# Performance work log

Hardware: AMD Instinct MI355X
Metric: run time of the kernel (lower is better)

## Reference

```python
import jax, jax.numpy as jnp
import numpy as np

BATCH = 16384
STEPS = 32
LAT = 64
IN_W = STEPS * (2 * LAT + 1) + 2 * LAT  # 4256


def setup_inputs() -> dict:
    key = jax.random.key(0)
    k1, k2 = jax.random.split(key)
    inputs = jax.random.normal(k1, (BATCH, IN_W), dtype=jnp.float32) * 0.1
    noise = jax.random.normal(k2, (BATCH, LAT), dtype=jnp.float32)
    return {"inputs": inputs, "noise": noise, "flow_steps": STEPS, "latent_dim": LAT}


def reference(inputs, noise, flow_steps, latent_dim):
    S, L = flow_steps, latent_dim
    B = inputs.shape[0]
    q0_mu = inputs[:, :L]
    q0_logsigma2 = inputs[:, L:2 * L]
    z0 = q0_mu + noise * jnp.exp(0.5 * q0_logsigma2)  # reparam sample (B, L)
    # initial variational loss term (add_loss in original)
    kl0 = -0.5 * jnp.mean(jnp.sum(noise * noise, axis=-1) + jnp.sum(q0_logsigma2, axis=-1))
    # per-step flow params, laid out step-major for scan: (S, B, L) and (S, B)
    U = inputs[:, 2 * L:(2 + S) * L].reshape(B, S, L).transpose(1, 0, 2)
    W = inputs[:, (2 + S) * L:(2 + 2 * S) * L].reshape(B, S, L).transpose(1, 0, 2)
    b = inputs[:, (2 + 2 * S) * L:(2 + 2 * S) * L + S].T  # (S, B)

    def step(z, uwb):
        u, w, bb = uwb
        h = jnp.sum(w * z, axis=-1) + bb          # (B,)
        uw = jnp.sum(u * w, axis=-1)              # (B,)
        t = jnp.tanh(h)
        # log|det Jacobian| loss term (tanh activation branch)
        loss = -jnp.mean(jnp.log(jnp.abs((1.0 - t * t) * uw + 1.0)))
        z = z + u * t[:, None]
        return z, loss

    z, losses = jax.lax.scan(step, z0, (U, W, b))
    total_loss = kl0 + jnp.sum(losses)
    return z, total_loss
```

## Files before the change

kernel.cpp:

```cpp
#include <hip/hip_runtime.h>
#include <math.h>


constexpr int BATCH = 16384;
constexpr int STEPS = 32;
constexpr int LAT   = 64;
constexpr int IN_W  = STEPS * (2 * LAT + 1) + 2 * LAT;

template <int CTRL>
__device__ __forceinline__ float dpp_mov(float x) {
    return __int_as_float(
        __builtin_amdgcn_update_dpp(0, __float_as_int(x), CTRL, 0xF, 0xF, true));
}

__device__ __forceinline__ float wave_reduce_to63(float x) {
    x += dpp_mov<0x111>(x);
    x += dpp_mov<0x112>(x);
    x += dpp_mov<0x114>(x);
    x += dpp_mov<0x118>(x);
    x += dpp_mov<0x142>(x);
    x += dpp_mov<0x143>(x);
    return x;
}

__device__ __forceinline__ float bcast63(float x) {
    return __int_as_float(__builtin_amdgcn_readlane(__float_as_int(x), 63));
}

__global__ __launch_bounds__(256)
void planar_flow_kernel(const float* __restrict__ inputs,
                        const float* __restrict__ noise,
                        float* __restrict__ z_out,
                        float* __restrict__ loss_out)
{
    const int lane = threadIdx.x & 63;
    const int wv   = threadIdx.x >> 6;
    const int row  = (blockIdx.x << 2) + wv;

    const float* rp = inputs + (size_t)row * IN_W;

    float mu  = rp[lane];
    float ls2 = rp[LAT + lane];
    float nz  = noise[(size_t)row * LAT + lane];
    float bvec = rp[2 * LAT + 2 * STEPS * LAT + (lane & 31)];

    float z = mu + nz * __expf(0.5f * ls2);

    float kl = wave_reduce_to63(nz * nz + ls2);
    float acc = -0.5f * kl;

    const float* up = rp + 2 * LAT;
    const float* wp = rp + 2 * LAT + STEPS * LAT;

    #pragma unroll 8
    for (int s = 0; s < STEPS; ++s) {
        float u = up[s * LAT + lane];
        float w = wp[s * LAT + lane];

        float hv = wave_reduce_to63(w * z);
        float bs = __int_as_float(__builtin_amdgcn_readlane(__float_as_int(bvec), s));
        float h  = bcast63(hv) + bs;

        float uwv = wave_reduce_to63(u * w);

        float e = __expf(2.0f * h);
        float t = 1.0f - 2.0f * __builtin_amdgcn_rcpf(e + 1.0f);

        acc -= __logf(fabsf((1.0f - t * t) * uwv + 1.0f));

        z += u * t;
    }

    z_out[(size_t)row * LAT + lane] = z;

    __shared__ float partial[4];
    if (lane == 63) partial[wv] = acc;
    __syncthreads();
    if (threadIdx.x == 0) {
        float s = (partial[0] + partial[1] + partial[2] + partial[3]) * (1.0f / BATCH);
        atomicAdd(loss_out, s);
    }
}

extern "C" void kernel_launch(void* const* d_in, const int* in_sizes, int n_in,
                              void* d_out, int out_size, void* d_ws, size_t ws_size,
                              hipStream_t stream)
{
    const float* inputs = (const float*)d_in[0];
    const float* noise  = (const float*)d_in[1];
    float* z_out    = (float*)d_out;
    float* loss_out = (float*)d_out + (size_t)BATCH * LAT;

    hipMemsetAsync(loss_out, 0, sizeof(float), stream);

    planar_flow_kernel<<<dim3(BATCH / 4), dim3(256), 0, stream>>>(
        inputs, noise, z_out, loss_out);
}
```

Before: 384.2 us.

## Map four rows per wavefront with float4 loads and 16-lane DPP reductions

Each wavefront now processes four batch rows, with 16 lanes per row and each lane owning four latent elements loaded as float4. Dot products are partially summed per lane, then reduced across 16 lanes with row-level DPP butterflies, so the readlane broadcasts go away and the bias is read from memory per step. This cuts the number of cross-lane reduction steps and widens memory transactions. The risk is reduced parallelism, with a quarter of the blocks, and the scalar bias load per step.

```diff
diff --git a/kernel.cpp b/kernel.cpp
--- a/kernel.cpp
+++ b/kernel.cpp
@@ -13,18 +13,12 @@
         __builtin_amdgcn_update_dpp(0, __float_as_int(x), CTRL, 0xF, 0xF, true));
 }
 
-__device__ __forceinline__ float wave_reduce_to63(float x) {
-    x += dpp_mov<0x111>(x);
-    x += dpp_mov<0x112>(x);
-    x += dpp_mov<0x114>(x);
-    x += dpp_mov<0x118>(x);
-    x += dpp_mov<0x142>(x);
-    x += dpp_mov<0x143>(x);
+__device__ __forceinline__ float red16(float x) {
+    x += dpp_mov<0x128>(x);
+    x += dpp_mov<0x124>(x);
+    x += dpp_mov<0x4E>(x);
+    x += dpp_mov<0xB1>(x);
     return x;
-}
-
-__device__ __forceinline__ float bcast63(float x) {
-    return __int_as_float(__builtin_amdgcn_readlane(__float_as_int(x), 63));
 }
 
 __global__ __launch_bounds__(256)
@@ -33,52 +27,63 @@
                         float* __restrict__ z_out,
                         float* __restrict__ loss_out)
 {
-    const int lane = threadIdx.x & 63;
-    const int wv   = threadIdx.x >> 6;
-    const int row  = (blockIdx.x << 2) + wv;
+    const int lane  = threadIdx.x & 63;
+    const int wv    = threadIdx.x >> 6;
+    const int group = lane >> 4;
+    const int li    = lane & 15;
+    const int row   = blockIdx.x * 16 + wv * 4 + group;
 
     const float* rp = inputs + (size_t)row * IN_W;
 
-    float mu  = rp[lane];
-    float ls2 = rp[LAT + lane];
-    float nz  = noise[(size_t)row * LAT + lane];
-    float bvec = rp[2 * LAT + 2 * STEPS * LAT + (lane & 31)];
+    float4 mu  = *(const float4*)(rp + 4 * li);
+    float4 ls2 = *(const float4*)(rp + LAT + 4 * li);
+    float4 nz  = *(const float4*)(noise + (size_t)row * LAT + 4 * li);
 
-    float z = mu + nz * __expf(0.5f * ls2);
+    float4 z;
+    z.x = mu.x + nz.x * __expf(0.5f * ls2.x);
+    z.y = mu.y + nz.y * __expf(0.5f * ls2.y);
+    z.z = mu.z + nz.z * __expf(0.5f * ls2.z);
+    z.w = mu.w + nz.w * __expf(0.5f * ls2.w);
 
-    float kl = wave_reduce_to63(nz * nz + ls2);
-    float acc = -0.5f * kl;
+    float klp = nz.x * nz.x + nz.y * nz.y + nz.z * nz.z + nz.w * nz.w
+              + ls2.x + ls2.y + ls2.z + ls2.w;
+    float acc = -0.5f * red16(klp);
 
     const float* up = rp + 2 * LAT;
     const float* wp = rp + 2 * LAT + STEPS * LAT;
+    const float* bp = rp + 2 * LAT + 2 * STEPS * LAT;
 
     #pragma unroll 8
     for (int s = 0; s < STEPS; ++s) {
-        float u = up[s * LAT + lane];
-        float w = wp[s * LAT + lane];
+        float4 u = *(const float4*)(up + s * LAT + 4 * li);
+        float4 w = *(const float4*)(wp + s * LAT + 4 * li);
+        float bs = bp[s];
 
-        float hv = wave_reduce_to63(w * z);
-        float bs = __int_as_float(__builtin_amdgcn_readlane(__float_as_int(bvec), s));
-        float h  = bcast63(hv) + bs;
+        float wz = w.x * z.x + w.y * z.y + w.z * z.z + w.w * z.w;
+        float uw = u.x * w.x + u.y * w.y + u.z * w.z + u.w * w.w;
+        if (li == 0) wz += bs;
 
-        float uwv = wave_reduce_to63(u * w);
+        wz = red16(wz);
+        uw = red16(uw);
 
-        float e = __expf(2.0f * h);
+        float e = __expf(2.0f * wz);
         float t = 1.0f - 2.0f * __builtin_amdgcn_rcpf(e + 1.0f);
 
-        acc -= __logf(fabsf((1.0f - t * t) * uwv + 1.0f));
+        acc -= __logf(fabsf((1.0f - t * t) * uw + 1.0f));
 
-        z += u * t;
+        z.x += u.x * t; z.y += u.y * t; z.z += u.z * t; z.w += u.w * t;
     }
 
-    z_out[(size_t)row * LAT + lane] = z;
+    *(float4*)(z_out + (size_t)row * LAT + 4 * li) = z;
 
-    __shared__ float partial[4];
-    if (lane == 63) partial[wv] = acc;
+    __shared__ float partial[16];
+    if (li == 0) partial[wv * 4 + group] = acc;
     __syncthreads();
     if (threadIdx.x == 0) {
-        float s = (partial[0] + partial[1] + partial[2] + partial[3]) * (1.0f / BATCH);
-        atomicAdd(loss_out, s);
+        float s = 0.0f;
+        #pragma unroll
+        for (int i = 0; i < 16; ++i) s += partial[i];
+        atomicAdd(loss_out, s * (1.0f / BATCH));
     }
 }
 
@@ -93,6 +98,6 @@
 
     hipMemsetAsync(loss_out, 0, sizeof(float), stream);
 
-    planar_flow_kernel<<<dim3(BATCH / 4), dim3(256), 0, stream>>>(
+    planar_flow_kernel<<<dim3(BATCH / 16), dim3(256), 0, stream>>>(
         inputs, noise, z_out, loss_out);
 }
```

Measured after the change: 388.4 us. About the same (+1.1%).
